# Performance work log

Hardware: AMD Instinct MI355X
Metric: run time of the kernel (lower is better)

The kernel has to match this reference:

```python
import jax, jax.numpy as jnp
import numpy as np

N_NODES = 10242  # icosphere level-5 node count
NNZ = 71694      # ~7 nonzeros per row (6 neighbors + self)


def setup_inputs() -> dict:
    key = jax.random.key(0)
    k1, k2, k3, k4, k5 = jax.random.split(key, 5)
    B, T, C, Cout, Ks = 2, 16, 16, 32, 20
    x = jax.random.normal(k1, (B, T, N_NODES, C), dtype=jnp.float32)
    edge_row = jax.random.randint(k2, (NNZ,), 0, N_NODES, dtype=jnp.int32)
    edge_col = jax.random.randint(k3, (NNZ,), 0, N_NODES, dtype=jnp.int32)
    # small values keep the Chebyshev recurrence numerically bounded over Ks steps
    edge_val = jax.random.uniform(k4, (NNZ,), dtype=jnp.float32, minval=-0.2, maxval=0.2)
    W = jax.random.normal(k5, (Cout, C * Ks), dtype=jnp.float32) * 0.02
    return {"x": x, "edge_row": edge_row, "edge_col": edge_col,
            "edge_val": edge_val, "W": W}


def reference(x, edge_row, edge_col, edge_val, W):
    B, T, N, C = x.shape
    Cout, CK = W.shape
    Ks = CK // C

    def spmm(v):  # sparse L @ v, v: [N, F]
        return jax.ops.segment_sum(edge_val[:, None] * v[edge_col], edge_row,
                                   num_segments=N)

    # [B,T,N,C] -> [B*T,N,C] -> [N,C,B*T] -> [N, C*B*T]
    x0 = x.reshape(B * T, N, C).transpose(1, 2, 0).reshape(N, C * B * T)
    x1 = spmm(x0)

    def step(carry, _):
        a, b = carry
        c = 2.0 * spmm(b) - a
        return (b, c), c

    _, rest = jax.lax.scan(step, (x0, x1), None, length=Ks - 2)
    xs = jnp.concatenate([x0[None], x1[None], rest], axis=0)  # [Ks, N, C*B*T]

    xs = xs.reshape(Ks, N, C, B * T).transpose(3, 1, 2, 0)  # [B*T, N, C, Ks]
    xs = xs.reshape(B * T * N, C * Ks)
    out = xs @ W.T  # [B*T*N, Cout]
    return out.reshape(B, T, N, Cout)
```

## Files before the change

kernel.cpp:

```cpp
#include <hip/hip_runtime.h>

#define N_NODES 10242
#define NNZ_E   71694
#define NNZ_PAD_MAX (NNZ_E + 3 * N_NODES)
#define BT      32
#define C_IN    16
#define K_S     20
#define C_OUT   32
#define F       512
typedef unsigned short u16;
typedef unsigned int   u32;

#define RING_ELEMS ((size_t)N_NODES * F)
#define RING_BYTES (RING_ELEMS * 2)
#define R_SLOTS    8

typedef __attribute__((ext_vector_type(8)))  _Float16 half8;
typedef __attribute__((ext_vector_type(16))) float    float16;

__device__ __forceinline__ void unpack8h(uint4 u, float* f) {
    union { uint4 u; _Float16 h[8]; } v; v.u = u;
    #pragma unroll
    for (int i = 0; i < 8; ++i) f[i] = (float)v.h[i];
}
__device__ __forceinline__ uint4 pack8h(const float* f) {
    union { uint4 u; _Float16 h[8]; } v;
    #pragma unroll
    for (int i = 0; i < 8; ++i) v.h[i] = (_Float16)f[i];
    return v.u;
}
__device__ __forceinline__ u16 f2h(float f) {
    union { _Float16 h; u16 u; } v; v.h = (_Float16)f; return v.u;
}


__global__ void zero_kernel(int* p, int n) {
    int i = blockIdx.x * blockDim.x + threadIdx.x;
    if (i < n) p[i] = 0;
}

__global__ void count_kernel(const int* __restrict__ erow, int* cnt) {
    int e = blockIdx.x * blockDim.x + threadIdx.x;
    if (e < NNZ_E) atomicAdd(&cnt[erow[e]], 1);
}

__global__ void scan_kernel(const int* __restrict__ cnt, int* row_ptr, int* cursor) {
    const int T = 256;
    const int chunk = (N_NODES + T - 1) / T;
    __shared__ int part[T];
    int t = threadIdx.x;
    int base = t * chunk;
    int s = 0;
    for (int i = 0; i < chunk; ++i) {
        int idx = base + i;
        if (idx < N_NODES) s += (cnt[idx] + 3) & ~3;
    }
    part[t] = s;
    __syncthreads();
    for (int off = 1; off < T; off <<= 1) {
        int v = (t >= off) ? part[t - off] : 0;
        __syncthreads();
        part[t] += v;
        __syncthreads();
    }
    int run = (t == 0) ? 0 : part[t - 1];
    for (int i = 0; i < chunk; ++i) {
        int idx = base + i;
        if (idx < N_NODES) {
            row_ptr[idx] = run;
            cursor[idx]  = run;
            run += (cnt[idx] + 3) & ~3;
        }
    }
    if (base <= N_NODES && N_NODES < base + chunk) {
        row_ptr[N_NODES] = run;
    }
}

__global__ void scatter_kernel(const int* __restrict__ erow, int* cursor, int* __restrict__ eidx) {
    int e = blockIdx.x * blockDim.x + threadIdx.x;
    if (e < NNZ_E) {
        int p = atomicAdd(&cursor[erow[e]], 1);
        eidx[p] = e;
    }
}

__global__ void sort_rows_kernel(const int* __restrict__ row_ptr, const int* __restrict__ cnt,
                                 int* eidx) {
    int r = blockIdx.x * blockDim.x + threadIdx.x;
    if (r >= N_NODES) return;
    int s = row_ptr[r], e = s + cnt[r];
    for (int i = s + 1; i < e; ++i) {
        int key = eidx[i];
        int j = i - 1;
        while (j >= s && eidx[j] > key) { eidx[j + 1] = eidx[j]; --j; }
        eidx[j + 1] = key;
    }
}

__global__ void fill_csr_kernel(const int* __restrict__ row_ptr, const int* __restrict__ cnt,
                                const int* __restrict__ eidx,
                                const int* __restrict__ ecol, const float* __restrict__ eval,
                                int2* __restrict__ cpack) {
    int r = blockIdx.x * blockDim.x + threadIdx.x;
    if (r >= N_NODES) return;
    int s = row_ptr[r], e = s + cnt[r];
    for (int p = s; p < e; ++p) {
        int ed = eidx[p];
        cpack[p] = make_int2(ecol[ed], __float_as_int(eval[ed]));
    }
}

__global__ void wtfrag_kernel(const float* __restrict__ W, u16* __restrict__ wtfrag) {
    int i = blockIdx.x * blockDim.x + threadIdx.x;
    if (i >= K_S * 64 * 8) return;
    int j    = i & 7;
    int lane = (i >> 3) & 63;
    int k    = i >> 9;
    int cout = lane & 31;
    int c    = ((lane >> 5) << 3) + j;
    wtfrag[i] = f2h(W[cout * (C_IN * K_S) + c * K_S + k]);
}


__global__ __launch_bounds__(256) void transform_kernel(
        const float* __restrict__ x, u16* __restrict__ T0) {
    int g = blockIdx.x * 256 + threadIdx.x;
    int n   = g >> 9;
    int rem = g & 511;
    int bt  = rem >> 4;
    int c   = rem & 15;
    float v = x[((size_t)bt * N_NODES + n) * C_IN + c];
    T0[(size_t)n * F + rem] = f2h(v);
}


__global__ __launch_bounds__(64) void spmm_step_kernel(
        const u16* __restrict__ srcB, const u16* __restrict__ srcA,
        u16* __restrict__ dst,
        const int* __restrict__ row_ptr, const int2* __restrict__ cpack,
        float alpha, float beta) {
    int n = blockIdx.x;
    int lane = threadIdx.x;
    int s = row_ptr[n], e_end = row_ptr[n + 1];

    float a[8] = {0,0,0,0,0,0,0,0};
    if (beta != 0.f) {
        uint4 ua = ((const uint4*)(srcA + (size_t)n * F))[lane];
        unpack8h(ua, a);
    }

    float acc0[8] = {0,0,0,0,0,0,0,0};
    float acc1[8] = {0,0,0,0,0,0,0,0};

    for (int e = s; e < e_end; e += 4) {
        int2 p0 = cpack[e + 0], p1 = cpack[e + 1];
        int2 p2 = cpack[e + 2], p3 = cpack[e + 3];
        uint4 g0 = ((const uint4*)(srcB + (size_t)p0.x * F))[lane];
        uint4 g1 = ((const uint4*)(srcB + (size_t)p1.x * F))[lane];
        uint4 g2 = ((const uint4*)(srcB + (size_t)p2.x * F))[lane];
        uint4 g3 = ((const uint4*)(srcB + (size_t)p3.x * F))[lane];
        float b0[8], b1[8], b2[8], b3[8];
        unpack8h(g0, b0); unpack8h(g1, b1); unpack8h(g2, b2); unpack8h(g3, b3);
        float v0 = __int_as_float(p0.y), v1 = __int_as_float(p1.y);
        float v2 = __int_as_float(p2.y), v3 = __int_as_float(p3.y);
        #pragma unroll
        for (int i = 0; i < 8; ++i) {
            acc0[i] += v0 * b0[i];
            acc1[i] += v1 * b1[i];
            acc0[i] += v2 * b2[i];
            acc1[i] += v3 * b3[i];
        }
    }

    float y[8];
    #pragma unroll
    for (int i = 0; i < 8; ++i)
        y[i] = alpha * (acc0[i] + acc1[i]) + beta * a[i];

    ((uint4*)(dst + (size_t)n * F))[lane] = pack8h(y);
}


__global__ __launch_bounds__(256) void proj_mfma_kernel(
        const u16* __restrict__ ring, int k0, int kcnt,
        const u16* __restrict__ wtfrag, float* __restrict__ out, int accumulate) {
    int wave = threadIdx.x >> 6;
    int lane = threadIdx.x & 63;
    int n = blockIdx.x * 4 + wave;
    if (n >= N_NODES) return;

    int col = lane & 31;
    int grp = lane >> 5;
    size_t aoff = (size_t)n * F + (size_t)col * 16 + grp * 8;

    union { uint4 u; half8 h; } av[8], bv[8];
    #pragma unroll
    for (int j = 0; j < 8; ++j) {
        int jj = (j < kcnt) ? j : 0;
        int k = k0 + jj;
        av[j].u = *(const uint4*)(ring + (size_t)(k % R_SLOTS) * RING_ELEMS + aoff);
        bv[j].u = *(const uint4*)(wtfrag + (size_t)k * 512 + lane * 8);
    }

    float16 acc = {};
    #pragma unroll
    for (int j = 0; j < 8; ++j) {
        if (j < kcnt)
            acc = __builtin_amdgcn_mfma_f32_32x32x16_f16(av[j].h, bv[j].h, acc, 0, 0, 0);
    }

    #pragma unroll
    for (int r = 0; r < 16; ++r) {
        int bt = (r & 3) + 8 * (r >> 2) + 4 * grp;
        float* op = out + ((size_t)bt * N_NODES + n) * C_OUT + col;
        if (accumulate) *op += acc[r];
        else            *op  = acc[r];
    }
}


extern "C" void kernel_launch(void* const* d_in, const int* in_sizes, int n_in,
                              void* d_out, int out_size, void* d_ws, size_t ws_size,
                              hipStream_t stream) {
    const float* x    = (const float*)d_in[0];
    const int*   erow = (const int*)  d_in[1];
    const int*   ecol = (const int*)  d_in[2];
    const float* eval = (const float*)d_in[3];
    const float* W    = (const float*)d_in[4];
    float* out = (float*)d_out;

    char* ws = (char*)d_ws;
    size_t o = 0;
    auto alloc = [&](size_t bytes) -> char* {
        o = (o + 511) & ~(size_t)511;
        char* r = ws + o;
        o += bytes;
        return r;
    };
    int*   cnt     = (int*)  alloc((size_t)N_NODES * 4);
    int*   row_ptr = (int*)  alloc((size_t)(N_NODES + 1) * 4);
    int*   cursor  = (int*)  alloc((size_t)N_NODES * 4);
    int*   eidx    = (int*)  alloc((size_t)NNZ_PAD_MAX * 4);
    int2*  cpack   = (int2*) alloc((size_t)NNZ_PAD_MAX * 8);
    u16*   wtfrag  = (u16*)  alloc((size_t)K_S * 512 * 2);

    u16* ring = (u16*)alloc((size_t)R_SLOTS * RING_BYTES);
    auto slot = [&](int k) -> u16* { return ring + (size_t)(k % R_SLOTS) * RING_ELEMS; };

    zero_kernel<<<(N_NODES + 255) / 256, 256, 0, stream>>>(cnt, N_NODES);
    zero_kernel<<<(2 * NNZ_PAD_MAX + 255) / 256, 256, 0, stream>>>((int*)cpack, 2 * NNZ_PAD_MAX);
    count_kernel<<<(NNZ_E + 255) / 256, 256, 0, stream>>>(erow, cnt);
    scan_kernel<<<1, 256, 0, stream>>>(cnt, row_ptr, cursor);
    scatter_kernel<<<(NNZ_E + 255) / 256, 256, 0, stream>>>(erow, cursor, eidx);
    sort_rows_kernel<<<(N_NODES + 255) / 256, 256, 0, stream>>>(row_ptr, cnt, eidx);
    fill_csr_kernel<<<(N_NODES + 255) / 256, 256, 0, stream>>>(row_ptr, cnt, eidx, ecol, eval, cpack);
    wtfrag_kernel<<<(K_S * 512 + 255) / 256, 256, 0, stream>>>(W, wtfrag);

    const int proj_blocks = (N_NODES + 3) / 4;
    int c0 = 0;
    auto maybe_pass = [&](int k_done) {
        int target = K_S - c0;
        if (target > R_SLOTS) target = R_SLOTS;
        if (target > 0 && (k_done - c0 + 1) == target) {
            proj_mfma_kernel<<<proj_blocks, 256, 0, stream>>>(
                ring, c0, target, wtfrag, out, (c0 > 0) ? 1 : 0);
            c0 += target;
        }
    };

    transform_kernel<<<(int)(RING_ELEMS / 256), 256, 0, stream>>>(x, slot(0));
    maybe_pass(0);

    for (int k = 1; k < K_S; ++k) {
        const u16* srcB = slot(k - 1);
        const u16* srcA = (k >= 2) ? slot(k - 2) : slot(k - 1);
        float alpha = (k == 1) ? 1.f : 2.f;
        float beta  = (k == 1) ? 0.f : -1.f;
        spmm_step_kernel<<<N_NODES, 64, 0, stream>>>(
            srcB, srcA, slot(k), row_ptr, cpack, alpha, beta);
        maybe_pass(k);
    }
}
```

Baseline: 493.0 us.

## Fuse CSR build into one kernel, broadcast edges via readlane, size ring dynamically

```diff
diff --git a/kernel.cpp b/kernel.cpp
--- a/kernel.cpp
+++ b/kernel.cpp
@@ -2,7 +2,7 @@
 
 #define N_NODES 10242
 #define NNZ_E   71694
-#define NNZ_PAD_MAX (NNZ_E + 3 * N_NODES)
+#define NNZ_PAD_MAX (NNZ_E + 7 * N_NODES + 64)
 #define BT      32
 #define C_IN    16
 #define K_S     20
@@ -13,7 +13,6 @@
 
 #define RING_ELEMS ((size_t)N_NODES * F)
 #define RING_BYTES (RING_ELEMS * 2)
-#define R_SLOTS    8
 
 typedef __attribute__((ext_vector_type(8)))  _Float16 half8;
 typedef __attribute__((ext_vector_type(16))) float    float16;
@@ -34,92 +33,83 @@
 }
 
 
-__global__ void zero_kernel(int* p, int n) {
-    int i = blockIdx.x * blockDim.x + threadIdx.x;
-    if (i < n) p[i] = 0;
-}
-
-__global__ void count_kernel(const int* __restrict__ erow, int* cnt) {
-    int e = blockIdx.x * blockDim.x + threadIdx.x;
-    if (e < NNZ_E) atomicAdd(&cnt[erow[e]], 1);
-}
-
-__global__ void scan_kernel(const int* __restrict__ cnt, int* row_ptr, int* cursor) {
-    const int T = 256;
-    const int chunk = (N_NODES + T - 1) / T;
-    __shared__ int part[T];
-    int t = threadIdx.x;
-    int base = t * chunk;
-    int s = 0;
-    for (int i = 0; i < chunk; ++i) {
-        int idx = base + i;
-        if (idx < N_NODES) s += (cnt[idx] + 3) & ~3;
-    }
-    part[t] = s;
-    __syncthreads();
-    for (int off = 1; off < T; off <<= 1) {
+__global__ __launch_bounds__(1024) void build_kernel(
+        const int* __restrict__ erow, const int* __restrict__ ecol,
+        const float* __restrict__ eval, const float* __restrict__ W,
+        int* __restrict__ row_ptr, int2* __restrict__ cpack,
+        u16* __restrict__ wtfrag) {
+    __shared__ int cnt[N_NODES];
+    __shared__ int cur[N_NODES];
+    __shared__ int part[1024];
+    const int t = threadIdx.x;
+
+    for (int i = t; i < K_S * 64 * 8; i += 1024) {
+        int j    = i & 7;
+        int lane = (i >> 3) & 63;
+        int k    = i >> 9;
+        int cout = lane & 31;
+        int c    = ((lane >> 5) << 3) + j;
+        wtfrag[i] = f2h(W[cout * (C_IN * K_S) + c * K_S + k]);
+    }
+
+    for (int i = t; i < N_NODES; i += 1024) cnt[i] = 0;
+    __syncthreads();
+    for (int e = t; e < NNZ_E; e += 1024) atomicAdd(&cnt[erow[e]], 1);
+    __syncthreads();
+
+    const int CH = (N_NODES + 1023) / 1024;
+    int b0 = t * CH;
+    int sloc = 0;
+    for (int i = 0; i < CH; ++i) {
+        int idx = b0 + i;
+        if (idx < N_NODES) sloc += (cnt[idx] + 7) & ~7;
+    }
+    part[t] = sloc;
+    __syncthreads();
+    for (int off = 1; off < 1024; off <<= 1) {
         int v = (t >= off) ? part[t - off] : 0;
         __syncthreads();
         part[t] += v;
         __syncthreads();
     }
     int run = (t == 0) ? 0 : part[t - 1];
-    for (int i = 0; i < chunk; ++i) {
-        int idx = base + i;
+    for (int i = 0; i < CH; ++i) {
+        int idx = b0 + i;
         if (idx < N_NODES) {
+            cur[idx]     = run;
             row_ptr[idx] = run;
-            cursor[idx]  = run;
-            run += (cnt[idx] + 3) & ~3;
+            run += (cnt[idx] + 7) & ~7;
         }
     }
-    if (base <= N_NODES && N_NODES < base + chunk) {
-        row_ptr[N_NODES] = run;
-    }
-}
-
-__global__ void scatter_kernel(const int* __restrict__ erow, int* cursor, int* __restrict__ eidx) {
-    int e = blockIdx.x * blockDim.x + threadIdx.x;
-    if (e < NNZ_E) {
-        int p = atomicAdd(&cursor[erow[e]], 1);
-        eidx[p] = e;
-    }
-}
-
-__global__ void sort_rows_kernel(const int* __restrict__ row_ptr, const int* __restrict__ cnt,
-                                 int* eidx) {
-    int r = blockIdx.x * blockDim.x + threadIdx.x;
-    if (r >= N_NODES) return;
-    int s = row_ptr[r], e = s + cnt[r];
-    for (int i = s + 1; i < e; ++i) {
-        int key = eidx[i];
-        int j = i - 1;
-        while (j >= s && eidx[j] > key) { eidx[j + 1] = eidx[j]; --j; }
-        eidx[j + 1] = key;
-    }
-}
-
-__global__ void fill_csr_kernel(const int* __restrict__ row_ptr, const int* __restrict__ cnt,
-                                const int* __restrict__ eidx,
-                                const int* __restrict__ ecol, const float* __restrict__ eval,
-                                int2* __restrict__ cpack) {
-    int r = blockIdx.x * blockDim.x + threadIdx.x;
-    if (r >= N_NODES) return;
-    int s = row_ptr[r], e = s + cnt[r];
-    for (int p = s; p < e; ++p) {
-        int ed = eidx[p];
-        cpack[p] = make_int2(ecol[ed], __float_as_int(eval[ed]));
-    }
-}
-
-__global__ void wtfrag_kernel(const float* __restrict__ W, u16* __restrict__ wtfrag) {
-    int i = blockIdx.x * blockDim.x + threadIdx.x;
-    if (i >= K_S * 64 * 8) return;
-    int j    = i & 7;
-    int lane = (i >> 3) & 63;
-    int k    = i >> 9;
-    int cout = lane & 31;
-    int c    = ((lane >> 5) << 3) + j;
-    wtfrag[i] = f2h(W[cout * (C_IN * K_S) + c * K_S + k]);
+    if (t == 1023) row_ptr[N_NODES] = part[1023];
+    __syncthreads();
+
+    for (int e = t; e < NNZ_E; e += 1024) {
+        int r = erow[e];
+        int p = atomicAdd(&cur[r], 1);
+        cpack[p] = make_int2(ecol[e], __float_as_int(eval[e]));
+    }
+    __syncthreads();
+
+    for (int r = t; r < N_NODES; r += 1024) {
+        int c    = cnt[r];
+        int send = cur[r];
+        int sbeg = send - c;
+        for (int i = sbeg + 1; i < send; ++i) {
+            int2 key = cpack[i];
+            int j = i - 1;
+            while (j >= sbeg) {
+                int2 q = cpack[j];
+                bool gt = (q.x > key.x) || (q.x == key.x && (u32)q.y > (u32)key.y);
+                if (!gt) break;
+                cpack[j + 1] = q;
+                --j;
+            }
+            cpack[j + 1] = key;
+        }
+        int pend = sbeg + ((c + 7) & ~7);
+        for (int p = send; p < pend; ++p) cpack[p] = make_int2(0, 0);
+    }
 }
 
 
@@ -135,14 +125,15 @@
 }
 
 
-__global__ __launch_bounds__(64) void spmm_step_kernel(
+__global__ __launch_bounds__(256) void spmm_step_kernel(
         const u16* __restrict__ srcB, const u16* __restrict__ srcA,
         u16* __restrict__ dst,
         const int* __restrict__ row_ptr, const int2* __restrict__ cpack,
         float alpha, float beta) {
-    int n = blockIdx.x;
-    int lane = threadIdx.x;
-    int s = row_ptr[n], e_end = row_ptr[n + 1];
+    const int lane = threadIdx.x & 63;
+    const int n = (blockIdx.x << 2) + (threadIdx.x >> 6);
+    if (n >= N_NODES) return;
+    const int s = row_ptr[n], e_end = row_ptr[n + 1];
 
     float a[8] = {0,0,0,0,0,0,0,0};
     if (beta != 0.f) {
@@ -150,26 +141,53 @@
         unpack8h(ua, a);
     }
 
+    int2 my = cpack[s + lane];
+
     float acc0[8] = {0,0,0,0,0,0,0,0};
     float acc1[8] = {0,0,0,0,0,0,0,0};
 
-    for (int e = s; e < e_end; e += 4) {
-        int2 p0 = cpack[e + 0], p1 = cpack[e + 1];
-        int2 p2 = cpack[e + 2], p3 = cpack[e + 3];
-        uint4 g0 = ((const uint4*)(srcB + (size_t)p0.x * F))[lane];
-        uint4 g1 = ((const uint4*)(srcB + (size_t)p1.x * F))[lane];
-        uint4 g2 = ((const uint4*)(srcB + (size_t)p2.x * F))[lane];
-        uint4 g3 = ((const uint4*)(srcB + (size_t)p3.x * F))[lane];
-        float b0[8], b1[8], b2[8], b3[8];
+    for (int e = s; e < e_end; e += 8) {
+        const int base = e - s;
+        int c0 = __builtin_amdgcn_readlane(my.x, base + 0);
+        int c1 = __builtin_amdgcn_readlane(my.x, base + 1);
+        int c2 = __builtin_amdgcn_readlane(my.x, base + 2);
+        int c3 = __builtin_amdgcn_readlane(my.x, base + 3);
+        int c4 = __builtin_amdgcn_readlane(my.x, base + 4);
+        int c5 = __builtin_amdgcn_readlane(my.x, base + 5);
+        int c6 = __builtin_amdgcn_readlane(my.x, base + 6);
+        int c7 = __builtin_amdgcn_readlane(my.x, base + 7);
+        float v0 = __int_as_float(__builtin_amdgcn_readlane(my.y, base + 0));
+        float v1 = __int_as_float(__builtin_amdgcn_readlane(my.y, base + 1));
+        float v2 = __int_as_float(__builtin_amdgcn_readlane(my.y, base + 2));
+        float v3 = __int_as_float(__builtin_amdgcn_readlane(my.y, base + 3));
+        float v4 = __int_as_float(__builtin_amdgcn_readlane(my.y, base + 4));
+        float v5 = __int_as_float(__builtin_amdgcn_readlane(my.y, base + 5));
+        float v6 = __int_as_float(__builtin_amdgcn_readlane(my.y, base + 6));
+        float v7 = __int_as_float(__builtin_amdgcn_readlane(my.y, base + 7));
+
+        uint4 g0 = ((const uint4*)(srcB + (size_t)c0 * F))[lane];
+        uint4 g1 = ((const uint4*)(srcB + (size_t)c1 * F))[lane];
+        uint4 g2 = ((const uint4*)(srcB + (size_t)c2 * F))[lane];
+        uint4 g3 = ((const uint4*)(srcB + (size_t)c3 * F))[lane];
+        uint4 g4 = ((const uint4*)(srcB + (size_t)c4 * F))[lane];
+        uint4 g5 = ((const uint4*)(srcB + (size_t)c5 * F))[lane];
+        uint4 g6 = ((const uint4*)(srcB + (size_t)c6 * F))[lane];
+        uint4 g7 = ((const uint4*)(srcB + (size_t)c7 * F))[lane];
+
+        float b0[8], b1[8], b2[8], b3[8], b4[8], b5[8], b6[8], b7[8];
         unpack8h(g0, b0); unpack8h(g1, b1); unpack8h(g2, b2); unpack8h(g3, b3);
-        float v0 = __int_as_float(p0.y), v1 = __int_as_float(p1.y);
-        float v2 = __int_as_float(p2.y), v3 = __int_as_float(p3.y);
+        unpack8h(g4, b4); unpack8h(g5, b5); unpack8h(g6, b6); unpack8h(g7, b7);
+
         #pragma unroll
         for (int i = 0; i < 8; ++i) {
             acc0[i] += v0 * b0[i];
             acc1[i] += v1 * b1[i];
             acc0[i] += v2 * b2[i];
             acc1[i] += v3 * b3[i];
+            acc0[i] += v4 * b4[i];
+            acc1[i] += v5 * b5[i];
+            acc0[i] += v6 * b6[i];
+            acc1[i] += v7 * b7[i];
         }
     }
 
@@ -183,39 +201,44 @@
 
 
 __global__ __launch_bounds__(256) void proj_mfma_kernel(
-        const u16* __restrict__ ring, int k0, int kcnt,
+        const u16* __restrict__ ring, int R, int k0, int kcnt,
         const u16* __restrict__ wtfrag, float* __restrict__ out, int accumulate) {
-    int wave = threadIdx.x >> 6;
-    int lane = threadIdx.x & 63;
-    int n = blockIdx.x * 4 + wave;
+    const int lane = threadIdx.x & 63;
+    const int n = (blockIdx.x << 2) + (threadIdx.x >> 6);
     if (n >= N_NODES) return;
-
-    int col = lane & 31;
-    int grp = lane >> 5;
-    size_t aoff = (size_t)n * F + (size_t)col * 16 + grp * 8;
-
-    union { uint4 u; half8 h; } av[8], bv[8];
-    #pragma unroll
-    for (int j = 0; j < 8; ++j) {
-        int jj = (j < kcnt) ? j : 0;
-        int k = k0 + jj;
-        av[j].u = *(const uint4*)(ring + (size_t)(k % R_SLOTS) * RING_ELEMS + aoff);
-        bv[j].u = *(const uint4*)(wtfrag + (size_t)k * 512 + lane * 8);
-    }
-
-    float16 acc = {};
-    #pragma unroll
-    for (int j = 0; j < 8; ++j) {
-        if (j < kcnt)
-            acc = __builtin_amdgcn_mfma_f32_32x32x16_f16(av[j].h, bv[j].h, acc, 0, 0, 0);
+    const int col = lane & 31;
+    const int grp = lane >> 5;
+    const size_t aoff = (size_t)n * F + (size_t)col * 16 + grp * 8;
+
+    union U { uint4 u; half8 h; };
+    float16 acc0 = {};
+    float16 acc1 = {};
+    int j = 0;
+    for (; j + 2 <= kcnt; j += 2) {
+        int ka = k0 + j, kb = k0 + j + 1;
+        U a0, b0, a1, b1;
+        a0.u = *(const uint4*)(ring + (size_t)(ka % R) * RING_ELEMS + aoff);
+        b0.u = *(const uint4*)(wtfrag + (size_t)ka * 512 + lane * 8);
+        a1.u = *(const uint4*)(ring + (size_t)(kb % R) * RING_ELEMS + aoff);
+        b1.u = *(const uint4*)(wtfrag + (size_t)kb * 512 + lane * 8);
+        acc0 = __builtin_amdgcn_mfma_f32_32x32x16_f16(a0.h, b0.h, acc0, 0, 0, 0);
+        acc1 = __builtin_amdgcn_mfma_f32_32x32x16_f16(a1.h, b1.h, acc1, 0, 0, 0);
+    }
+    if (j < kcnt) {
+        int ka = k0 + j;
+        U a0, b0;
+        a0.u = *(const uint4*)(ring + (size_t)(ka % R) * RING_ELEMS + aoff);
+        b0.u = *(const uint4*)(wtfrag + (size_t)ka * 512 + lane * 8);
+        acc0 = __builtin_amdgcn_mfma_f32_32x32x16_f16(a0.h, b0.h, acc0, 0, 0, 0);
     }
 
     #pragma unroll
     for (int r = 0; r < 16; ++r) {
         int bt = (r & 3) + 8 * (r >> 2) + 4 * grp;
         float* op = out + ((size_t)bt * N_NODES + n) * C_OUT + col;
-        if (accumulate) *op += acc[r];
-        else            *op  = acc[r];
+        float val = acc0[r] + acc1[r];
+        if (accumulate) *op += val;
+        else            *op  = val;
     }
 }
 
@@ -238,33 +261,27 @@
         o += bytes;
         return r;
     };
-    int*   cnt     = (int*)  alloc((size_t)N_NODES * 4);
     int*   row_ptr = (int*)  alloc((size_t)(N_NODES + 1) * 4);
-    int*   cursor  = (int*)  alloc((size_t)N_NODES * 4);
-    int*   eidx    = (int*)  alloc((size_t)NNZ_PAD_MAX * 4);
     int2*  cpack   = (int2*) alloc((size_t)NNZ_PAD_MAX * 8);
     u16*   wtfrag  = (u16*)  alloc((size_t)K_S * 512 * 2);
 
-    u16* ring = (u16*)alloc((size_t)R_SLOTS * RING_BYTES);
-    auto slot = [&](int k) -> u16* { return ring + (size_t)(k % R_SLOTS) * RING_ELEMS; };
-
-    zero_kernel<<<(N_NODES + 255) / 256, 256, 0, stream>>>(cnt, N_NODES);
-    zero_kernel<<<(2 * NNZ_PAD_MAX + 255) / 256, 256, 0, stream>>>((int*)cpack, 2 * NNZ_PAD_MAX);
-    count_kernel<<<(NNZ_E + 255) / 256, 256, 0, stream>>>(erow, cnt);
-    scan_kernel<<<1, 256, 0, stream>>>(cnt, row_ptr, cursor);
-    scatter_kernel<<<(NNZ_E + 255) / 256, 256, 0, stream>>>(erow, cursor, eidx);
-    sort_rows_kernel<<<(N_NODES + 255) / 256, 256, 0, stream>>>(row_ptr, cnt, eidx);
-    fill_csr_kernel<<<(N_NODES + 255) / 256, 256, 0, stream>>>(row_ptr, cnt, eidx, ecol, eval, cpack);
-    wtfrag_kernel<<<(K_S * 512 + 255) / 256, 256, 0, stream>>>(W, wtfrag);
-
-    const int proj_blocks = (N_NODES + 3) / 4;
+    o = (o + 511) & ~(size_t)511;
+    int R = (int)((ws_size - o) / RING_BYTES);
+    if (R > K_S) R = K_S;
+    if (R < 3)  R = 3;
+    u16* ring = (u16*)(ws + o);
+    auto slot = [&](int k) -> u16* { return ring + (size_t)(k % R) * RING_ELEMS; };
+
+    build_kernel<<<1, 1024, 0, stream>>>(erow, ecol, eval, W, row_ptr, cpack, wtfrag);
+
+    const int grid4 = (N_NODES + 3) / 4;
     int c0 = 0;
     auto maybe_pass = [&](int k_done) {
         int target = K_S - c0;
-        if (target > R_SLOTS) target = R_SLOTS;
+        if (target > R) target = R;
         if (target > 0 && (k_done - c0 + 1) == target) {
-            proj_mfma_kernel<<<proj_blocks, 256, 0, stream>>>(
-                ring, c0, target, wtfrag, out, (c0 > 0) ? 1 : 0);
+            proj_mfma_kernel<<<grid4, 256, 0, stream>>>(
+                ring, R, c0, target, wtfrag, out, (c0 > 0) ? 1 : 0);
             c0 += target;
         }
     };
@@ -277,7 +294,7 @@
         const u16* srcA = (k >= 2) ? slot(k - 2) : slot(k - 1);
         float alpha = (k == 1) ? 1.f : 2.f;
         float beta  = (k == 1) ? 0.f : -1.f;
-        spmm_step_kernel<<<N_NODES, 64, 0, stream>>>(
+        spmm_step_kernel<<<grid4, 256, 0, stream>>>(
             srcB, srcA, slot(k), row_ptr, cpack, alpha, beta);
         maybe_pass(k);
     }
```

Result: slower. 878.7 us (+78.2%).
